# Kernel tuning notes

Hardware: AMD Instinct MI355X
Metric: run time of the kernel (lower is better)

## Reference

```python
import jax, jax.numpy as jnp
import numpy as np

SCALING = 32.0 / 16.0  # alpha / r


def setup_inputs() -> dict:
    key = jax.random.key(0)
    ks = jax.random.split(key, 6)
    B, S, IN, OUT, R = 4, 2048, 4096, 4096, 16
    x = jax.random.normal(ks[0], (B, S, IN), dtype=jnp.float32)
    # packed 4-bit weights: each int holds two nibbles (values 0..255)
    qweight = jax.random.randint(ks[1], (OUT, IN // 2), 0, 256, dtype=jnp.int32)
    scales = (jax.random.uniform(ks[2], (OUT,), dtype=jnp.float32) * 0.01 + 1e-4).astype(jnp.float16)
    zeros = (jax.random.normal(ks[3], (OUT,), dtype=jnp.float32) * 0.05).astype(jnp.float16)
    lora_A = jax.random.normal(ks[4], (R, IN), dtype=jnp.float32) * (1.0 / np.sqrt(IN))
    lora_B = jax.random.normal(ks[5], (OUT, R), dtype=jnp.float32) * 0.01
    return {"x": x, "qweight": qweight, "scales": scales, "zeros": zeros,
            "lora_A": lora_A, "lora_B": lora_B}


def _dequantize(qweight, scales, zeros):
    # qweight: [O, I//2] packed bytes -> high nibble goes to even cols, low to odd
    high = (qweight >> 4).astype(jnp.float32)          # [O, I//2]
    low = (qweight & 15).astype(jnp.float32)           # [O, I//2]
    O, half = qweight.shape
    w = jnp.stack([high, low], axis=-1).reshape(O, half * 2)  # interleave -> [O, I]
    return w * scales.astype(jnp.float32)[:, None] + zeros.astype(jnp.float32)[:, None]


def reference(x, qweight, scales, zeros, lora_A, lora_B):
    W = _dequantize(qweight, scales, zeros)            # [O, I] fp32
    base = jnp.einsum('bsi,oi->bso', x, W)             # F.linear, no bias
    lora = jnp.einsum('bsi,ri->bsr', x, lora_A)        # [B,S,r]
    lora = jnp.einsum('bsr,or->bso', lora, lora_B) * SCALING
    return base + lora
```

## Files before the change

kernel.cpp:

```cpp
#include <hip/hip_runtime.h>
#include <hip/hip_fp16.h>

#define MDIM 8192
#define NDIM 4096
#define KDIM 4096

typedef unsigned short u16;
typedef __bf16 bf16x8 __attribute__((ext_vector_type(8)));
typedef float f32x4 __attribute__((ext_vector_type(4)));

static __device__ __forceinline__ u16 f2bf(float f) {
  union { float f; unsigned u; } v; v.f = f;
  unsigned r = v.u + 0x7fffu + ((v.u >> 16) & 1u);
  return (u16)(r >> 16);
}

static __device__ __forceinline__ bool sz_is_f32(const void* sc) {
  unsigned w0 = ((const unsigned*)sc)[0];
  return ((w0 >> 16) & 0x7fffu) >= 0x3000u;
}
static __device__ __forceinline__ float load_sz(const void* p, int i, bool f32) {
  return f32 ? ((const float*)p)[i] : __half2float(((const __half*)p)[i]);
}

#define CONVB 2048
#define WEFFB 512
__global__ void qlora_prep(const float4* __restrict__ x, ushort4* __restrict__ xb,
                           const int* __restrict__ qw, const void* __restrict__ sc,
                           const void* __restrict__ zr, const float* __restrict__ lA,
                           const float* __restrict__ lB, ushort2* __restrict__ weff) {
  if (blockIdx.x < CONVB) {
    unsigned base = blockIdx.x * 256u + threadIdx.x;
#pragma unroll
    for (int s = 0; s < 16; ++s) {
      unsigned i = base + (unsigned)s * (CONVB * 256u);
      float4 a = x[i];
      ushort4 o;
      o.x = f2bf(a.x); o.y = f2bf(a.y); o.z = f2bf(a.z); o.w = f2bf(a.w);
      xb[i] = o;
    }
  } else {
    __shared__ __align__(16) float lA_s[16][512];
    __shared__ float lB_s[64][16];
    __shared__ float s_s[64], z_s[64];
    const int bid = blockIdx.x - CONVB;
    const int t = threadIdx.x;
    const int o0 = (bid & 63) * 64;
    const int it0 = (bid >> 6) * 512;
    const bool f32 = sz_is_f32(sc);
#pragma unroll
    for (int s = 0; s < 8; ++s) {
      int idx = s * 256 + t;
      int r = idx >> 7, c4 = idx & 127;
      *(float4*)&lA_s[r][c4 * 4] = *(const float4*)(lA + (size_t)r * KDIM + it0 + c4 * 4);
    }
#pragma unroll
    for (int s = 0; s < 4; ++s) {
      int idx = s * 256 + t;
      int o = idx >> 4, r = idx & 15;
      lB_s[o][r] = lB[(o0 + o) * 16 + r] * 2.0f;
    }
    if (t < 64) {
      s_s[t] = load_sz(sc, o0 + t, f32);
      z_s[t] = load_sz(zr, o0 + t, f32);
    }
    __syncthreads();
    float2 a2[16];
#pragma unroll
    for (int r = 0; r < 16; ++r) a2[r] = *(const float2*)&lA_s[r][2 * t];
    const size_t i2 = (size_t)(it0 / 2 + t);
    const int* qcol = qw + i2;
    ushort2* wcol = weff + i2;
#pragma unroll 4
    for (int o = 0; o < 64; ++o) {
      const int oo = o0 + o;
      int q = qcol[(size_t)oo * (KDIM / 2)];
      float acc0 = 0.f, acc1 = 0.f;
#pragma unroll
      for (int r = 0; r < 16; ++r) {
        float br = lB_s[o][r];
        acc0 += br * a2[r].x;
        acc1 += br * a2[r].y;
      }
      const float s = s_s[o], z = z_s[o];
      float w0 = (float)((q >> 4) & 15) * s + z + acc0;
      float w1 = (float)(q & 15) * s + z + acc1;
      ushort2 pk; pk.x = f2bf(w0); pk.y = f2bf(w1);
      wcol[(size_t)oo * (KDIM / 2)] = pk;
    }
  }
}


#define STAGE(SB, BUFSEL, REGOFF, HALF, KT) do {                                   \
    const u16* _s0 = (SB) + (size_t)(HALF) * (128 * (size_t)KDIM) + (KT) * 64;     \
    u16* _d0 = lds + (BUFSEL) * 32768 + (REGOFF) + (HALF) * 8192 + wave * 1024;    \
    __builtin_amdgcn_global_load_lds(                                              \
        (const __attribute__((address_space(1))) void*)_s0,                        \
        (__attribute__((address_space(3))) void*)_d0, 16, 0, 0);                   \
    __builtin_amdgcn_global_load_lds(                                              \
        (const __attribute__((address_space(1))) void*)(_s0 + 8 * KDIM),           \
        (__attribute__((address_space(3))) void*)(_d0 + 512), 16, 0, 0);           \
  } while (0)

#define VMW2 asm volatile("s_waitcnt vmcnt(2)" ::: "memory")

#define PHASE(BUF, QM, KK, LOADB, STAGE_STMT, VM_STMT) do {                        \
    __builtin_amdgcn_sched_barrier(0);                                            \
    bf16x8 af[4];                                                                 \
    {                                                                             \
      int _ab = (BUF) * 32768 + (QM) * 8192 + aRowBase;                           \
      if (KK) _ab ^= 32;                                                          \
      _Pragma("unroll")                                                           \
      for (int mf = 0; mf < 4; ++mf)                                              \
        af[mf] = *(const bf16x8*)(lds + (_ab + mf * 1024));                       \
      if (LOADB) {                                                                \
        int _bb = (BUF) * 32768 + bRowBase;                                       \
        if (KK) _bb ^= 32;                                                        \
        _Pragma("unroll")                                                         \
        for (int nf = 0; nf < 4; ++nf)                                            \
          bfr[nf][KK] = *(const bf16x8*)(lds + (_bb + nf * 1024));                \
      }                                                                           \
    }                                                                             \
    STAGE_STMT;                                                                   \
    __builtin_amdgcn_sched_barrier(0);                                            \
    __builtin_amdgcn_s_barrier();                                                 \
    asm volatile("s_waitcnt lgkmcnt(0)" ::: "memory");                            \
    __builtin_amdgcn_sched_barrier(0);                                            \
    __builtin_amdgcn_s_setprio(1);                                                \
    _Pragma("unroll")                                                             \
    for (int mf = 0; mf < 4; ++mf)                                                \
      _Pragma("unroll")                                                           \
      for (int nf = 0; nf < 4; ++nf)                                              \
        acc[QM][mf][nf] = __builtin_amdgcn_mfma_f32_16x16x32_bf16(                \
            af[mf], bfr[nf][KK], acc[QM][mf][nf], 0, 0, 0);                       \
    __builtin_amdgcn_s_setprio(0);                                                \
    VM_STMT;                                                                      \
    __builtin_amdgcn_sched_barrier(0);                                            \
    __builtin_amdgcn_s_barrier();                                                 \
  } while (0)

__global__ __launch_bounds__(512, 2) void qlora_gemm8p(const u16* __restrict__ A,
                                                       const u16* __restrict__ B,
                                                       float* __restrict__ C) {
  __shared__ __align__(16) u16 lds[65536];

  const int t = threadIdx.x;
  const int lane = t & 63;
  const int wave = t >> 6;
  const int wr = wave >> 2;
  const int wc = wave & 3;
  const int lrow = lane & 15;
  const int khalf = lane >> 4;
  const int g0 = (khalf ^ (lane & 7)) * 8;

  const int flat = blockIdx.x;
  const int xcd = flat & 7;
  const int idx = flat >> 3;
  const int brow = ((xcd & 3) * 8 + (idx & 7)) * 256;
  const int bcol = ((xcd >> 2) * 8 + (idx >> 3)) * 256;

  const int aRowBase = (wr * 64 + lrow) * 64 + g0;
  const int bRowBase = 16384 + (wc * 64 + lrow) * 64 + g0;

  const int srow = wave * 16 + (lane >> 3);
  const int sg = ((lane & 7) ^ ((lane >> 3) & 7)) * 8;
  const u16* aS = A + (size_t)(brow + srow) * KDIM + sg;
  const u16* bS = B + (size_t)(bcol + srow) * KDIM + sg;

  f32x4 acc[2][4][4] = {};
  bf16x8 bfr[4][2];

  STAGE(aS, 0, 0, 0, 0);
  STAGE(aS, 0, 0, 1, 0);
  STAGE(bS, 0, 16384, 0, 0);
  STAGE(bS, 0, 16384, 1, 0);
  STAGE(aS, 1, 0, 0, 1);
  asm volatile("s_waitcnt vmcnt(2)" ::: "memory");
  __builtin_amdgcn_s_barrier();

#pragma unroll 1
  for (int it = 0; it < KDIM / 128; ++it) {
    const int o1 = 2 * it + 1;
    const int e2 = (2 * it + 2) & 63;
    const int o3 = (2 * it + 3) & 63;
    PHASE(0, 0, 0, 1, STAGE(aS, 1, 0, 1, o1), );
    PHASE(0, 0, 1, 1, STAGE(bS, 1, 16384, 0, o1), );
    PHASE(0, 1, 0, 0, STAGE(bS, 1, 16384, 1, o1), );
    PHASE(0, 1, 1, 0, STAGE(aS, 0, 0, 0, e2), VMW2);
    PHASE(1, 0, 0, 1, STAGE(aS, 0, 0, 1, e2), );
    PHASE(1, 0, 1, 1, STAGE(bS, 0, 16384, 0, e2), );
    PHASE(1, 1, 0, 0, STAGE(bS, 0, 16384, 1, e2), );
    PHASE(1, 1, 1, 0, STAGE(aS, 1, 0, 0, o3), VMW2);
  }

  asm volatile("s_waitcnt vmcnt(0) lgkmcnt(0)" ::: "memory");

  float* Cb = C + (size_t)brow * NDIM + bcol;
  const int rb = wr * 64 + (lane >> 4) * 4;
  const int cb = wc * 64 + lrow;
#pragma unroll
  for (int qm = 0; qm < 2; ++qm)
#pragma unroll
    for (int mf = 0; mf < 4; ++mf)
#pragma unroll
      for (int nf = 0; nf < 4; ++nf) {
        const int r = qm * 128 + rb + mf * 16;
        const int c = cb + nf * 16;
        f32x4 v = acc[qm][mf][nf];
#pragma unroll
        for (int q = 0; q < 4; ++q)
          Cb[(size_t)(r + q) * NDIM + c] = v[q];
      }
}

__global__ void qlora_fallback(const float* __restrict__ X, const int* __restrict__ qw,
                               const void* __restrict__ sc, const void* __restrict__ zr,
                               const float* __restrict__ lA, const float* __restrict__ lB,
                               float* __restrict__ C) {
  __shared__ float Xs[32][65];
  __shared__ float Ws[32][65];
  const int t = threadIdx.x;
  const bool f32 = sz_is_f32(sc);
  const int brow = blockIdx.x * 64, bcol = blockIdx.y * 64;
  const int tr = t >> 4, tc = t & 15;
  float acc[4][4] = {};
  for (int k0 = 0; k0 < KDIM; k0 += 32) {
    __syncthreads();
    {
      int row = t >> 2;
      int kk0 = (t & 3) * 8;
      const float* src = X + (size_t)(brow + row) * KDIM + k0 + kk0;
#pragma unroll
      for (int u = 0; u < 8; ++u) Xs[kk0 + u][row] = src[u];
    }
    {
      int o = t >> 2;
      int kk0 = (t & 3) * 8;
      int oo = bcol + o;
      float s = load_sz(sc, oo, f32), z = load_sz(zr, oo, f32);
      const int* qrow = qw + (size_t)oo * (KDIM / 2) + (k0 + kk0) / 2;
#pragma unroll
      for (int u = 0; u < 4; ++u) {
        int q = qrow[u];
        int kk = kk0 + u * 2;
        float l0 = 0.f, l1 = 0.f;
#pragma unroll
        for (int r = 0; r < 16; ++r) {
          float br = lB[oo * 16 + r] * 2.0f;
          l0 += br * lA[(size_t)r * KDIM + k0 + kk];
          l1 += br * lA[(size_t)r * KDIM + k0 + kk + 1];
        }
        Ws[kk][o] = (float)((q >> 4) & 15) * s + z + l0;
        Ws[kk + 1][o] = (float)(q & 15) * s + z + l1;
      }
    }
    __syncthreads();
#pragma unroll
    for (int k = 0; k < 32; ++k) {
      float xv[4], wv[4];
#pragma unroll
      for (int i = 0; i < 4; ++i) xv[i] = Xs[k][tr * 4 + i];
#pragma unroll
      for (int j = 0; j < 4; ++j) wv[j] = Ws[k][tc * 4 + j];
#pragma unroll
      for (int i = 0; i < 4; ++i)
#pragma unroll
        for (int j = 0; j < 4; ++j) acc[i][j] += xv[i] * wv[j];
    }
  }
#pragma unroll
  for (int i = 0; i < 4; ++i)
#pragma unroll
    for (int j = 0; j < 4; ++j)
      C[(size_t)(brow + tr * 4 + i) * NDIM + bcol + tc * 4 + j] = acc[i][j];
}

extern "C" void kernel_launch(void* const* d_in, const int* in_sizes, int n_in,
                              void* d_out, int out_size, void* d_ws, size_t ws_size,
                              hipStream_t stream) {
  const float* x = (const float*)d_in[0];
  const int* qw = (const int*)d_in[1];
  const void* sc = d_in[2];
  const void* zr = d_in[3];
  const float* lA = (const float*)d_in[4];
  const float* lB = (const float*)d_in[5];
  float* out = (float*)d_out;

  const size_t xb_bytes = (size_t)MDIM * KDIM * 2;
  const size_t weff_bytes = (size_t)NDIM * KDIM * 2;
  if (ws_size >= xb_bytes + weff_bytes) {
    u16* xb = (u16*)d_ws;
    u16* weff = xb + (size_t)MDIM * KDIM;
    qlora_prep<<<CONVB + WEFFB, 256, 0, stream>>>((const float4*)x, (ushort4*)xb,
                                                  qw, sc, zr, lA, lB, (ushort2*)weff);
    dim3 grid((MDIM / 256) * (NDIM / 256));
    qlora_gemm8p<<<grid, 512, 0, stream>>>(xb, weff, out);
  } else {
    dim3 grid(MDIM / 64, NDIM / 64);
    qlora_fallback<<<grid, 256, 0, stream>>>(x, qw, sc, zr, lA, lB, out);
  }
}
```

Before: 292.8 us.

## Cut GEMM workgroup barriers to one gate per two compute phases and deepen prefetch

```diff
diff --git a/kernel.cpp b/kernel.cpp
--- a/kernel.cpp
+++ b/kernel.cpp
@@ -103,46 +103,48 @@
         (__attribute__((address_space(3))) void*)(_d0 + 512), 16, 0, 0);           \
   } while (0)
 
-#define VMW2 asm volatile("s_waitcnt vmcnt(2)" ::: "memory")
-
-#define PHASE(BUF, QM, KK, LOADB, STAGE_STMT, VM_STMT) do {                        \
-    __builtin_amdgcn_sched_barrier(0);                                            \
-    bf16x8 af[4];                                                                 \
-    {                                                                             \
-      int _ab = (BUF) * 32768 + (QM) * 8192 + aRowBase;                           \
-      if (KK) _ab ^= 32;                                                          \
-      _Pragma("unroll")                                                           \
-      for (int mf = 0; mf < 4; ++mf)                                              \
-        af[mf] = *(const bf16x8*)(lds + (_ab + mf * 1024));                       \
-      if (LOADB) {                                                                \
-        int _bb = (BUF) * 32768 + bRowBase;                                       \
-        if (KK) _bb ^= 32;                                                        \
-        _Pragma("unroll")                                                         \
-        for (int nf = 0; nf < 4; ++nf)                                            \
-          bfr[nf][KK] = *(const bf16x8*)(lds + (_bb + nf * 1024));                \
-      }                                                                           \
-    }                                                                             \
-    STAGE_STMT;                                                                   \
-    __builtin_amdgcn_sched_barrier(0);                                            \
-    __builtin_amdgcn_s_barrier();                                                 \
-    asm volatile("s_waitcnt lgkmcnt(0)" ::: "memory");                            \
-    __builtin_amdgcn_sched_barrier(0);                                            \
-    __builtin_amdgcn_s_setprio(1);                                                \
-    _Pragma("unroll")                                                             \
-    for (int mf = 0; mf < 4; ++mf)                                                \
-      _Pragma("unroll")                                                           \
-      for (int nf = 0; nf < 4; ++nf)                                              \
-        acc[QM][mf][nf] = __builtin_amdgcn_mfma_f32_16x16x32_bf16(                \
-            af[mf], bfr[nf][KK], acc[QM][mf][nf], 0, 0, 0);                       \
-    __builtin_amdgcn_s_setprio(0);                                                \
-    VM_STMT;                                                                      \
-    __builtin_amdgcn_sched_barrier(0);                                            \
-    __builtin_amdgcn_s_barrier();                                                 \
+#define SBAR0 __builtin_amdgcn_sched_barrier(0)
+
+#define GATE(N) do {                                                               \
+    asm volatile("s_waitcnt vmcnt(" #N ")" ::: "memory");                          \
+    SBAR0;                                                                         \
+    __builtin_amdgcn_s_barrier();                                                  \
+    SBAR0;                                                                         \
   } while (0)
 
-__global__ __launch_bounds__(512, 2) void qlora_gemm8p(const u16* __restrict__ A,
-                                                       const u16* __restrict__ B,
-                                                       float* __restrict__ C) {
+#define COMPUTE(BUF, QM, KK, LOADB, STAGE_STMT) do {                               \
+    bf16x8 af[4];                                                                  \
+    {                                                                              \
+      int _ab = (BUF) * 32768 + (QM) * 8192 + aRowBase;                            \
+      if (KK) _ab ^= 32;                                                           \
+      _Pragma("unroll")                                                            \
+      for (int mf = 0; mf < 4; ++mf)                                               \
+        af[mf] = *(const bf16x8*)(lds + (_ab + mf * 1024));                        \
+      if (LOADB) {                                                                 \
+        int _bb = (BUF) * 32768 + bRowBase;                                        \
+        if (KK) _bb ^= 32;                                                         \
+        _Pragma("unroll")                                                          \
+        for (int nf = 0; nf < 4; ++nf)                                             \
+          bfr[nf][KK] = *(const bf16x8*)(lds + (_bb + nf * 1024));                 \
+      }                                                                            \
+    }                                                                              \
+    SBAR0;                                                                         \
+    STAGE_STMT;                                                                    \
+    SBAR0;                                                                         \
+    __builtin_amdgcn_s_setprio(1);                                                 \
+    _Pragma("unroll")                                                              \
+    for (int mf = 0; mf < 4; ++mf)                                                 \
+      _Pragma("unroll")                                                            \
+      for (int nf = 0; nf < 4; ++nf)                                               \
+        acc[QM][mf][nf] = __builtin_amdgcn_mfma_f32_16x16x32_bf16(                 \
+            af[mf], bfr[nf][KK], acc[QM][mf][nf], 0, 0, 0);                        \
+    __builtin_amdgcn_s_setprio(0);                                                 \
+    SBAR0;                                                                         \
+  } while (0)
+
+__global__ __launch_bounds__(512, 2) void qlora_gemm_sp(const u16* __restrict__ A,
+                                                        const u16* __restrict__ B,
+                                                        float* __restrict__ C) {
   __shared__ __align__(16) u16 lds[65536];
 
   const int t = threadIdx.x;
@@ -172,26 +174,31 @@
   bf16x8 bfr[4][2];
 
   STAGE(aS, 0, 0, 0, 0);
-  STAGE(aS, 0, 0, 1, 0);
   STAGE(bS, 0, 16384, 0, 0);
   STAGE(bS, 0, 16384, 1, 0);
+  STAGE(aS, 0, 0, 1, 0);
   STAGE(aS, 1, 0, 0, 1);
-  asm volatile("s_waitcnt vmcnt(2)" ::: "memory");
-  __builtin_amdgcn_s_barrier();
+  STAGE(bS, 1, 16384, 0, 1);
+  SBAR0;
 
 #pragma unroll 1
   for (int it = 0; it < KDIM / 128; ++it) {
     const int o1 = 2 * it + 1;
     const int e2 = (2 * it + 2) & 63;
     const int o3 = (2 * it + 3) & 63;
-    PHASE(0, 0, 0, 1, STAGE(aS, 1, 0, 1, o1), );
-    PHASE(0, 0, 1, 1, STAGE(bS, 1, 16384, 0, o1), );
-    PHASE(0, 1, 0, 0, STAGE(bS, 1, 16384, 1, o1), );
-    PHASE(0, 1, 1, 0, STAGE(aS, 0, 0, 0, e2), VMW2);
-    PHASE(1, 0, 0, 1, STAGE(aS, 0, 0, 1, e2), );
-    PHASE(1, 0, 1, 1, STAGE(bS, 0, 16384, 0, e2), );
-    PHASE(1, 1, 0, 0, STAGE(bS, 0, 16384, 1, e2), );
-    PHASE(1, 1, 1, 0, STAGE(aS, 1, 0, 0, o3), VMW2);
+
+    GATE(6);
+    COMPUTE(0, 0, 0, 1, STAGE(bS, 1, 16384, 1, o1));
+    COMPUTE(0, 0, 1, 1, STAGE(aS, 1, 0, 1, o1));
+    GATE(8);
+    COMPUTE(0, 1, 0, 0, STAGE(aS, 0, 0, 0, e2));
+    COMPUTE(0, 1, 1, 0, STAGE(bS, 0, 16384, 0, e2));
+    GATE(6);
+    COMPUTE(1, 0, 0, 1, STAGE(bS, 0, 16384, 1, e2));
+    COMPUTE(1, 0, 1, 1, STAGE(aS, 0, 0, 1, e2));
+    GATE(8);
+    COMPUTE(1, 1, 0, 0, STAGE(aS, 1, 0, 0, o3));
+    COMPUTE(1, 1, 1, 0, STAGE(bS, 1, 16384, 0, o3));
   }
 
   asm volatile("s_waitcnt vmcnt(0) lgkmcnt(0)" ::: "memory");
@@ -295,7 +302,7 @@
     qlora_prep<<<CONVB + WEFFB, 256, 0, stream>>>((const float4*)x, (ushort4*)xb,
                                                   qw, sc, zr, lA, lB, (ushort2*)weff);
     dim3 grid((MDIM / 256) * (NDIM / 256));
-    qlora_gemm8p<<<grid, 512, 0, stream>>>(xb, weff, out);
+    qlora_gemm_sp<<<grid, 512, 0, stream>>>(xb, weff, out);
   } else {
     dim3 grid(MDIM / 64, NDIM / 64);
     qlora_fallback<<<grid, 256, 0, stream>>>(x, qw, sc, zr, lA, lB, out);
```

Measured after the change: 288.4 us. About the same (-1.5%).
